# Performance work log

Hardware: AMD Instinct MI355X
Metric: run time of the kernel (lower is better)

The kernel has to match this reference:

```python
import jax, jax.numpy as jnp
import numpy as np

N_NODES = 50000
N_EDGES = 600000
D = 128
LN_EPS = 1e-5


def setup_inputs() -> dict:
    key = jax.random.key(0)
    ks = jax.random.split(key, 10)
    s = 1.0 / np.sqrt(D)
    return {
        "node_reps": jax.random.normal(ks[0], (N_NODES, D), jnp.float32),
        "edge_reps": jax.random.normal(ks[1], (N_EDGES, D), jnp.float32),
        "src_idx": jax.random.randint(ks[2], (N_EDGES,), 0, N_NODES, jnp.int32),
        "dst_idx": jnp.sort(jax.random.randint(ks[3], (N_EDGES,), 0, N_NODES, jnp.int32)),
        "Wq": jax.random.normal(ks[4], (D, D), jnp.float32) * s,
        "Wk": jax.random.normal(ks[5], (D, D), jnp.float32) * s,
        "Wv": jax.random.normal(ks[6], (D, D), jnp.float32) * s,
        "Wo": jax.random.normal(ks[7], (D, D), jnp.float32) * s,
        "ln_gamma": jnp.ones((D,), jnp.float32),
        "ln_beta": jnp.zeros((D,), jnp.float32),
        "W1": jax.random.normal(ks[8], (3 * D, D), jnp.float32) * (1.0 / np.sqrt(3 * D)),
        "b1": jnp.zeros((D,), jnp.float32),
        "W2": jax.random.normal(ks[9], (D, D), jnp.float32) * s,
        "b2": jnp.zeros((D,), jnp.float32),
    }


def _layer_norm(x, g, b):
    mu = jnp.mean(x, axis=-1, keepdims=True)
    var = jnp.mean(jnp.square(x - mu), axis=-1, keepdims=True)
    return (x - mu) * jax.lax.rsqrt(var + LN_EPS) * g + b


def reference(node_reps, edge_reps, src_idx, dst_idx, Wq, Wk, Wv, Wo,
              ln_gamma, ln_beta, W1, b1, W2, b2):
    n_nodes, d = node_reps.shape
    # dense projections once per node (kernel-friendly GEMMs)
    q = node_reps @ Wq                                  # [N, d]
    k_nodes = node_reps @ Wk                            # [N, d]
    v_nodes = node_reps @ Wv                            # [N, d]
    # per-edge gather + edge bias
    k_e = k_nodes[src_idx] + edge_reps                  # [E, d]
    scores = jnp.sum(q[dst_idx] * k_e, axis=-1) / jnp.sqrt(jnp.float32(d))  # [E]
    # segment softmax over edges sharing the same dst node
    seg_max = jax.ops.segment_max(scores, dst_idx, num_segments=n_nodes)
    ex = jnp.exp(scores - seg_max[dst_idx])
    denom = jax.ops.segment_sum(ex, dst_idx, num_segments=n_nodes)
    alpha = ex / denom[dst_idx]                          # [E]
    v_e = v_nodes[src_idx] + edge_reps                   # [E, d]
    agg = jax.ops.segment_sum(alpha[:, None] * v_e, dst_idx, num_segments=n_nodes)  # [N, d]
    updated = _layer_norm(node_reps + agg @ Wo, ln_gamma, ln_beta)  # [N, d]
    # triplet fusion MLP over (dst node, edge, src node)
    h_trip = jnp.concatenate([node_reps[dst_idx], edge_reps, node_reps[src_idx]], axis=-1)  # [E, 3d]
    fused = jax.nn.relu(h_trip @ W1 + b1) @ W2 + b2      # [E, d]
    return updated, fused
```

## Files before the change

### kernel.cpp

```cpp
#include <hip/hip_runtime.h>
#include <hip/hip_bf16.h>

#define NN 50000
#define NE 600000
#define D 128

typedef __bf16 bf16x8 __attribute__((ext_vector_type(8)));
typedef __bf16 bf16x4 __attribute__((ext_vector_type(4)));
typedef float f32x4 __attribute__((ext_vector_type(4)));


static __device__ __forceinline__ f32x4 bf4_to_f32(bf16x4 v) {
  f32x4 r;
  r[0] = (float)v[0]; r[1] = (float)v[1]; r[2] = (float)v[2]; r[3] = (float)v[3];
  return r;
}

static __device__ __forceinline__ void gload_lds16(const void* g, void* l) {
  __builtin_amdgcn_global_load_lds(
      (const __attribute__((address_space(1))) unsigned int*)g,
      (__attribute__((address_space(3))) unsigned int*)l, 16, 0, 0);
}

static __device__ __forceinline__ bf16x8 load_a_frag_nc(const float* __restrict__ A,
                                                        int row, int k0) {
  const f32x4* p = (const f32x4*)(A + (size_t)row * D + k0);
  f32x4 v0 = p[0], v1 = p[1];
  bf16x8 r;
  r[0] = (__bf16)v0[0]; r[1] = (__bf16)v0[1]; r[2] = (__bf16)v0[2]; r[3] = (__bf16)v0[3];
  r[4] = (__bf16)v1[0]; r[5] = (__bf16)v1[1]; r[6] = (__bf16)v1[2]; r[7] = (__bf16)v1[3];
  return r;
}

static __device__ __forceinline__ void stage_a_tile(const float* __restrict__ A, int M,
                                                    int row_base, char* lds, int tid) {
  const int l32 = tid & 31;
  const int g = tid >> 5;
#pragma unroll
  for (int it = 0; it < 16; ++it) {
    int rl = it * 8 + g;
    int r = row_base + rl;
    f32x4 v = {};
    if (r < M) v = *(const f32x4*)(A + (size_t)r * D + l32 * 4);
    bf16x4 b;
    b[0] = (__bf16)v[0]; b[1] = (__bf16)v[1]; b[2] = (__bf16)v[2]; b[3] = (__bf16)v[3];
    int byte = (rl * 256 + l32 * 8) ^ ((rl & 7) << 4);
    *(bf16x4*)(lds + byte) = b;
  }
}

static __device__ __forceinline__ bf16x8 read_a_frag(const char* lds, int rl, int k0) {
  int byte = (rl * 256 + k0 * 2) ^ ((rl & 7) << 4);
  return *(const bf16x8*)(lds + byte);
}

struct PrepArgs {
  const float* W[8];
  __bf16* WT[8];
  const int* dst;
  int* offs;
};

__global__ void prep_all(PrepArgs pa) {
  int b = blockIdx.x;
  if (b < 512) {
    int w = b >> 6;
    int t = (b & 63) * 256 + threadIdx.x;
    int n = t & 127, k = t >> 7;
    pa.WT[w][n * 128 + k] = (__bf16)pa.W[w][k * 128 + n];
  } else {
    int n = (b - 512) * 256 + threadIdx.x;
    if (n > NN) return;
    int lo = 0, hi = NE;
    while (lo < hi) {
      int mid = (lo + hi) >> 1;
      if (pa.dst[mid] < n) lo = mid + 1; else hi = mid;
    }
    pa.offs[n] = lo;
  }
}

struct GemmBatch {
  const __bf16* BT[5];
  void* C[5];
  const float* bias[5];
  int bf16out[5];
};

__global__ __launch_bounds__(256) void gemm_k128_b(const float* __restrict__ A,
                                                   GemmBatch gb, int M) {
  __shared__ __align__(16) char atile[128 * 256];
  const int y = blockIdx.y;
  const __bf16* __restrict__ BT = gb.BT[y];
  const int tid = threadIdx.x;
  const int lane = tid & 63;
  const int wave = tid >> 6;
  const int wr = wave >> 1, wc = wave & 1;
  const int row0 = blockIdx.x * 128;
  const int col0 = wc * 64;
  const int lr = lane & 15;
  const int lk = (lane >> 4) << 3;

  stage_a_tile(A, M, row0, atile, tid);
  __syncthreads();

  f32x4 acc[4][4] = {};
#pragma unroll
  for (int kk = 0; kk < 4; ++kk) {
    const int k0 = kk * 32 + lk;
    bf16x8 a[4], b[4];
#pragma unroll
    for (int m = 0; m < 4; ++m) a[m] = read_a_frag(atile, wr * 64 + m * 16 + lr, k0);
#pragma unroll
    for (int n = 0; n < 4; ++n) b[n] = *(const bf16x8*)(BT + (size_t)(col0 + n * 16 + lr) * D + k0);
#pragma unroll
    for (int m = 0; m < 4; ++m)
#pragma unroll
      for (int n = 0; n < 4; ++n)
        acc[m][n] = __builtin_amdgcn_mfma_f32_16x16x32_bf16(a[m], b[n], acc[m][n], 0, 0, 0);
  }
  const int rr = (lane >> 4) * 4;
  float bv[4] = {0.f, 0.f, 0.f, 0.f};
  if (gb.bias[y]) {
#pragma unroll
    for (int n = 0; n < 4; ++n) bv[n] = gb.bias[y][col0 + n * 16 + lr];
  }
  if (gb.bf16out[y]) {
    __bf16* __restrict__ C = (__bf16*)gb.C[y];
#pragma unroll
    for (int m = 0; m < 4; ++m)
#pragma unroll
      for (int j = 0; j < 4; ++j) {
        int r = row0 + wr * 64 + m * 16 + rr + j;
        if (r < M) {
#pragma unroll
          for (int n = 0; n < 4; ++n)
            C[(size_t)r * D + col0 + n * 16 + lr] = (__bf16)(acc[m][n][j] + bv[n]);
        }
      }
  } else {
    float* __restrict__ C = (float*)gb.C[y];
#pragma unroll
    for (int m = 0; m < 4; ++m)
#pragma unroll
      for (int j = 0; j < 4; ++j) {
        int r = row0 + wr * 64 + m * 16 + rr + j;
        if (r < M) {
#pragma unroll
          for (int n = 0; n < 4; ++n)
            C[(size_t)r * D + col0 + n * 16 + lr] = acc[m][n][j] + bv[n];
        }
      }
  }
}

__global__ __launch_bounds__(256) void fused_edge_attn(
    const float* __restrict__ edge,
    const __bf16* __restrict__ W1bT,
    const __bf16* __restrict__ W2T,
    const __bf16* __restrict__ P1,
    const __bf16* __restrict__ P3,
    const int* __restrict__ dst,
    const int* __restrict__ src,
    const float* __restrict__ b2,
    float* __restrict__ out_fused,
    const float* __restrict__ Q,
    const __bf16* __restrict__ K,
    const __bf16* __restrict__ V,
    const int* __restrict__ offs,
    const __bf16* __restrict__ WoT,
    const float* __restrict__ noderep,
    const float* __restrict__ gamma,
    const float* __restrict__ beta,
    float* __restrict__ out_updated) {
  __shared__ __align__(16) char bufA[64 * 256];
  __shared__ __align__(16) char bufB[64 * 256];
  const int tid = threadIdx.x;
  const int grp = blockIdx.x / 5;
  const int role = blockIdx.x % 5;

  if (role >= 2) {
    const int ebi = grp * 3 + (role - 2);
    const int eb = ebi * 64;
    const int lane = tid & 63;
    const int wave = tid >> 6;
    const int wr = wave >> 1, wc = wave & 1;
    const int lr = lane & 15;
    const int lk = (lane >> 4) << 3;
    const int col0 = wc * 64;

    {
      const int gr = lane >> 4;
      const int slot = lane & 15;
      int di[4], si[4];
#pragma unroll
      for (int c = 0; c < 4; ++c) {
        int rl = wave * 16 + c * 4 + gr;
        di[c] = dst[eb + rl];
        si[c] = src[eb + rl];
      }
#pragma unroll
      for (int c = 0; c < 4; ++c) {
        int rl = wave * 16 + c * 4 + gr;
        int sb = (slot * 16) ^ ((rl & 7) << 4);
        gload_lds16((const char*)(P1 + (size_t)di[c] * D) + sb,
                    bufA + (wave * 16 + c * 4) * 256);
        gload_lds16((const char*)(P3 + (size_t)si[c] * D) + sb,
                    bufB + (wave * 16 + c * 4) * 256);
      }
    }

    f32x4 acc[2][4] = {};
#pragma unroll
    for (int kk = 0; kk < 4; ++kk) {
      const int k0 = kk * 32 + lk;
      bf16x8 a[2], b[4];
#pragma unroll
      for (int m = 0; m < 2; ++m) a[m] = load_a_frag_nc(edge, eb + wr * 32 + m * 16 + lr, k0);
#pragma unroll
      for (int n = 0; n < 4; ++n) b[n] = *(const bf16x8*)(W1bT + (size_t)(col0 + n * 16 + lr) * D + k0);
#pragma unroll
      for (int m = 0; m < 2; ++m)
#pragma unroll
        for (int n = 0; n < 4; ++n)
          acc[m][n] = __builtin_amdgcn_mfma_f32_16x16x32_bf16(a[m], b[n], acc[m][n], 0, 0, 0);
    }
    __syncthreads();

    const int rr = (lane >> 4) * 4;
#pragma unroll
    for (int m = 0; m < 2; ++m) {
#pragma unroll
      for (int j = 0; j < 4; ++j) {
        int rl = wr * 32 + m * 16 + rr + j;
#pragma unroll
        for (int n = 0; n < 4; ++n) {
          int c = col0 + n * 16 + lr;
          int byte = (rl * 256 + c * 2) ^ ((rl & 7) << 4);
          float g1 = (float)*(const __bf16*)(bufA + byte);
          float g3 = (float)*(const __bf16*)(bufB + byte);
          float v = fmaxf(acc[m][n][j] + g1 + g3, 0.f);
          *(__bf16*)(bufA + byte) = (__bf16)v;
        }
      }
    }
    __syncthreads();

    float b2v[4];
#pragma unroll
    for (int n = 0; n < 4; ++n) b2v[n] = b2[col0 + n * 16 + lr];
    f32x4 acc2[2][4] = {};
#pragma unroll
    for (int kk = 0; kk < 4; ++kk) {
      const int k0 = kk * 32 + lk;
      bf16x8 a[2], b[4];
#pragma unroll
      for (int m = 0; m < 2; ++m) a[m] = read_a_frag(bufA, wr * 32 + m * 16 + lr, k0);
#pragma unroll
      for (int n = 0; n < 4; ++n) b[n] = *(const bf16x8*)(W2T + (size_t)(col0 + n * 16 + lr) * D + k0);
#pragma unroll
      for (int m = 0; m < 2; ++m)
#pragma unroll
        for (int n = 0; n < 4; ++n)
          acc2[m][n] = __builtin_amdgcn_mfma_f32_16x16x32_bf16(a[m], b[n], acc2[m][n], 0, 0, 0);
    }
#pragma unroll
    for (int m = 0; m < 2; ++m)
#pragma unroll
      for (int j = 0; j < 4; ++j) {
        int rl = wr * 32 + m * 16 + rr + j;
        int e = eb + rl;
#pragma unroll
        for (int n = 0; n < 4; ++n) {
          int c = col0 + n * 16 + lr;
          out_fused[(size_t)e * D + c] = acc2[m][n][j] + b2v[n];
        }
      }
  } else {
    const int nw = tid >> 5;
    int node = (grp * 2 + role) * 8 + nw;
    int l32 = tid & 31;
    int s0 = offs[node], s1 = offs[node + 1];
    int cnt = s1 - s0;
    f32x4 q = *(const f32x4*)(Q + (size_t)node * D + l32 * 4);
    float m = -__builtin_inff(), l = 0.f;
    f32x4 a = {0.f, 0.f, 0.f, 0.f};

    int si0 = 0, si1 = 0;
    bf16x4 kb0 = {}, vb0 = {};
    f32x4 ee0 = {};
    if (cnt > 0) si0 = src[s0];
    if (cnt > 1) si1 = src[s0 + 1];
    if (cnt > 0) {
      kb0 = *(const bf16x4*)(K + (size_t)si0 * D + l32 * 4);
      vb0 = *(const bf16x4*)(V + (size_t)si0 * D + l32 * 4);
      ee0 = *(const f32x4*)(edge + (size_t)s0 * D + l32 * 4);
    }
    for (int i = 0; i < cnt; ++i) {
      int si2 = 0;
      if (i + 2 < cnt) si2 = src[s0 + i + 2];
      bf16x4 kb1 = {}, vb1 = {};
      f32x4 ee1 = {};
      if (i + 1 < cnt) {
        kb1 = *(const bf16x4*)(K + (size_t)si1 * D + l32 * 4);
        vb1 = *(const bf16x4*)(V + (size_t)si1 * D + l32 * 4);
        ee1 = *(const f32x4*)(edge + (size_t)(s0 + i + 1) * D + l32 * 4);
      }
      f32x4 kpe = bf4_to_f32(kb0) + ee0;
      float part = q[0] * kpe[0] + q[1] * kpe[1] + q[2] * kpe[2] + q[3] * kpe[3];
#pragma unroll
      for (int off = 16; off >= 1; off >>= 1) part += __shfl_xor(part, off, 64);
      float s = part * 0.08838834764831845f;
      float mn = fmaxf(m, s);
      float sc = __expf(m - mn);
      float w = __expf(s - mn);
      l = l * sc + w;
      f32x4 vpe = bf4_to_f32(vb0) + ee0;
      a[0] = a[0] * sc + w * vpe[0];
      a[1] = a[1] * sc + w * vpe[1];
      a[2] = a[2] * sc + w * vpe[2];
      a[3] = a[3] * sc + w * vpe[3];
      m = mn;
      si0 = si1; si1 = si2;
      kb0 = kb1; vb0 = vb1; ee0 = ee1;
    }
    float inv = l > 0.f ? 1.f / l : 0.f;
    f32x4 r;
    r[0] = a[0] * inv; r[1] = a[1] * inv; r[2] = a[2] * inv; r[3] = a[3] * inv;

    {
      bf16x4 rb;
      rb[0] = (__bf16)r[0]; rb[1] = (__bf16)r[1];
      rb[2] = (__bf16)r[2]; rb[3] = (__bf16)r[3];
      int byte = (nw * 256 + l32 * 8) ^ ((nw & 7) << 4);
      *(bf16x4*)(bufA + byte) = rb;
    }
    __syncthreads();

    {
      const int wave = tid >> 6;
      const int lane = tid & 63;
      const int lr = lane & 15;
      const int lk = (lane >> 4) << 3;
      f32x4 acc[2] = {};
#pragma unroll
      for (int kk = 0; kk < 4; ++kk) {
        int k0 = kk * 32 + lk;
        bf16x8 af = read_a_frag(bufA, lr, k0);
#pragma unroll
        for (int t = 0; t < 2; ++t) {
          int n = wave * 2 + t;
          bf16x8 b = *(const bf16x8*)(WoT + (size_t)(n * 16 + lr) * D + k0);
          acc[t] = __builtin_amdgcn_mfma_f32_16x16x32_bf16(af, b, acc[t], 0, 0, 0);
        }
      }
      float* xl = (float*)bufB;
      const int rr = (lane >> 4) * 4;
      if (rr < 8) {
#pragma unroll
        for (int t = 0; t < 2; ++t) {
          int n = wave * 2 + t;
#pragma unroll
          for (int j = 0; j < 4; ++j)
            xl[(rr + j) * 128 + n * 16 + lr] = acc[t][j];
        }
      }
    }
    __syncthreads();

    {
      const float* xl = (const float*)bufB;
      f32x4 xv = *(const f32x4*)(xl + nw * 128 + l32 * 4);
      f32x4 nv = *(const f32x4*)(noderep + (size_t)node * D + l32 * 4);
      float x0 = xv[0] + nv[0], x1 = xv[1] + nv[1];
      float x2 = xv[2] + nv[2], x3 = xv[3] + nv[3];
      float s = x0 + x1 + x2 + x3;
#pragma unroll
      for (int off = 16; off >= 1; off >>= 1) s += __shfl_xor(s, off, 64);
      float mu = s * (1.f / 128.f);
      float d0 = x0 - mu, d1 = x1 - mu, d2 = x2 - mu, d3 = x3 - mu;
      float vv = d0 * d0 + d1 * d1 + d2 * d2 + d3 * d3;
#pragma unroll
      for (int off = 16; off >= 1; off >>= 1) vv += __shfl_xor(vv, off, 64);
      float rstd = rsqrtf(vv * (1.f / 128.f) + 1e-5f);
      f32x4 g = *(const f32x4*)(gamma + l32 * 4);
      f32x4 bb = *(const f32x4*)(beta + l32 * 4);
      f32x4 o;
      o[0] = d0 * rstd * g[0] + bb[0];
      o[1] = d1 * rstd * g[1] + bb[1];
      o[2] = d2 * rstd * g[2] + bb[2];
      o[3] = d3 * rstd * g[3] + bb[3];
      *(f32x4*)(out_updated + (size_t)node * D + l32 * 4) = o;
    }
  }
}

extern "C" void kernel_launch(void* const* d_in, const int* in_sizes, int n_in,
                              void* d_out, int out_size, void* d_ws, size_t ws_size,
                              hipStream_t stream) {
  const float* node = (const float*)d_in[0];
  const float* edge = (const float*)d_in[1];
  const int* src = (const int*)d_in[2];
  const int* dst = (const int*)d_in[3];
  const float* Wq = (const float*)d_in[4];
  const float* Wk = (const float*)d_in[5];
  const float* Wv = (const float*)d_in[6];
  const float* Wo = (const float*)d_in[7];
  const float* gamma = (const float*)d_in[8];
  const float* beta = (const float*)d_in[9];
  const float* W1 = (const float*)d_in[10];
  const float* b1 = (const float*)d_in[11];
  const float* W2 = (const float*)d_in[12];
  const float* b2 = (const float*)d_in[13];

  float* out_updated = (float*)d_out;
  float* out_fused = (float*)d_out + (size_t)NN * D;

  char* ws = (char*)d_ws;
  size_t o = 0;
  auto take = [&](size_t bytes) {
    char* p = ws + o;
    o = (o + bytes + 255) & ~(size_t)255;
    return p;
  };
  int* offs = (int*)take((NN + 1) * sizeof(int));
  __bf16* WqT = (__bf16*)take(128 * 128 * 2);
  __bf16* WkT = (__bf16*)take(128 * 128 * 2);
  __bf16* WvT = (__bf16*)take(128 * 128 * 2);
  __bf16* WoT = (__bf16*)take(128 * 128 * 2);
  __bf16* W1aT = (__bf16*)take(128 * 128 * 2);
  __bf16* W1bT = (__bf16*)take(128 * 128 * 2);
  __bf16* W1cT = (__bf16*)take(128 * 128 * 2);
  __bf16* W2T = (__bf16*)take(128 * 128 * 2);
  float* Qb = (float*)take((size_t)NN * D * 4);
  __bf16* Kb = (__bf16*)take((size_t)NN * D * 2);
  __bf16* Vb = (__bf16*)take((size_t)NN * D * 2);
  __bf16* P1b = (__bf16*)take((size_t)NN * D * 2);
  __bf16* P3b = (__bf16*)take((size_t)NN * D * 2);

  PrepArgs pa;
  pa.W[0] = Wq; pa.WT[0] = WqT;
  pa.W[1] = Wk; pa.WT[1] = WkT;
  pa.W[2] = Wv; pa.WT[2] = WvT;
  pa.W[3] = Wo; pa.WT[3] = WoT;
  pa.W[4] = W1; pa.WT[4] = W1aT;
  pa.W[5] = W1 + 128 * 128; pa.WT[5] = W1bT;
  pa.W[6] = W1 + 256 * 128; pa.WT[6] = W1cT;
  pa.W[7] = W2; pa.WT[7] = W2T;
  pa.dst = dst; pa.offs = offs;
  prep_all<<<512 + (NN + 256) / 256, 256, 0, stream>>>(pa);

  int gnode = (NN + 127) / 128;
  GemmBatch gb;
  gb.BT[0] = WqT;  gb.C[0] = Qb;  gb.bias[0] = nullptr; gb.bf16out[0] = 0;
  gb.BT[1] = WkT;  gb.C[1] = Kb;  gb.bias[1] = nullptr; gb.bf16out[1] = 1;
  gb.BT[2] = WvT;  gb.C[2] = Vb;  gb.bias[2] = nullptr; gb.bf16out[2] = 1;
  gb.BT[3] = W1aT; gb.C[3] = P1b; gb.bias[3] = b1;      gb.bf16out[3] = 1;
  gb.BT[4] = W1cT; gb.C[4] = P3b; gb.bias[4] = nullptr; gb.bf16out[4] = 1;
  gemm_k128_b<<<dim3(gnode, 5), 256, 0, stream>>>(node, gb, NN);

  fused_edge_attn<<<15625, 256, 0, stream>>>(edge, W1bT, W2T, P1b, P3b, dst, src,
                                             b2, out_fused, Qb, Kb, Vb, offs,
                                             WoT, node, gamma, beta, out_updated);
}
```

Measured before the change: 428.8 us.

## Fuse projection GEMMs per row tile, interleave K/V, shrink edge tiles, drop softmax max

The projection GEMM now loops over all five weight matrices inside one block using a 64-row A tile, instead of using one grid slice per weight. This reuses the staged activations and cuts redundant A loads. K and V are written interleaved into one buffer so each edge needs a single 16-byte gather, and the fused edge kernel uses 32-edge tiles with a swizzled 4-role block mapping, launch bounds of 8 blocks per CU, and DPP-based warp reductions. The online softmax no longer tracks a running max and exponentiates raw scores. That is cheaper but can overflow if scores grow large.

```diff
diff --git a/kernel.cpp b/kernel.cpp
--- a/kernel.cpp
+++ b/kernel.cpp
@@ -9,12 +9,6 @@
 typedef __bf16 bf16x4 __attribute__((ext_vector_type(4)));
 typedef float f32x4 __attribute__((ext_vector_type(4)));
 
-
-static __device__ __forceinline__ f32x4 bf4_to_f32(bf16x4 v) {
-  f32x4 r;
-  r[0] = (float)v[0]; r[1] = (float)v[1]; r[2] = (float)v[2]; r[3] = (float)v[3];
-  return r;
-}
 
 static __device__ __forceinline__ void gload_lds16(const void* g, void* l) {
   __builtin_amdgcn_global_load_lds(
@@ -32,12 +26,12 @@
   return r;
 }
 
-static __device__ __forceinline__ void stage_a_tile(const float* __restrict__ A, int M,
-                                                    int row_base, char* lds, int tid) {
+static __device__ __forceinline__ void stage_a_tile64(const float* __restrict__ A, int M,
+                                                      int row_base, char* lds, int tid) {
   const int l32 = tid & 31;
   const int g = tid >> 5;
 #pragma unroll
-  for (int it = 0; it < 16; ++it) {
+  for (int it = 0; it < 8; ++it) {
     int rl = it * 8 + g;
     int r = row_base + rl;
     f32x4 v = {};
@@ -52,6 +46,20 @@
 static __device__ __forceinline__ bf16x8 read_a_frag(const char* lds, int rl, int k0) {
   int byte = (rl * 256 + k0 * 2) ^ ((rl & 7) << 4);
   return *(const bf16x8*)(lds + byte);
+}
+
+template <int CTRL>
+static __device__ __forceinline__ float dpp_add(float x) {
+  int v = __builtin_amdgcn_update_dpp(0, __float_as_int(x), CTRL, 0xf, 0xf, true);
+  return x + __int_as_float(v);
+}
+
+static __device__ __forceinline__ float red32(float x) {
+  x = dpp_add<0xB1>(x);
+  x = dpp_add<0x4E>(x);
+  x = dpp_add<0x124>(x);
+  x = dpp_add<0x128>(x);
+  return x + __shfl_xor(x, 16, 64);
 }
 
 struct PrepArgs {
@@ -84,77 +92,74 @@
   const __bf16* BT[5];
   void* C[5];
   const float* bias[5];
-  int bf16out[5];
+  int mode[5];
 };
 
 __global__ __launch_bounds__(256) void gemm_k128_b(const float* __restrict__ A,
                                                    GemmBatch gb, int M) {
-  __shared__ __align__(16) char atile[128 * 256];
-  const int y = blockIdx.y;
-  const __bf16* __restrict__ BT = gb.BT[y];
+  __shared__ __align__(16) char atile[64 * 256];
   const int tid = threadIdx.x;
   const int lane = tid & 63;
   const int wave = tid >> 6;
   const int wr = wave >> 1, wc = wave & 1;
-  const int row0 = blockIdx.x * 128;
+  const int row0 = blockIdx.x * 64;
   const int col0 = wc * 64;
   const int lr = lane & 15;
   const int lk = (lane >> 4) << 3;
-
-  stage_a_tile(A, M, row0, atile, tid);
+  const int rr = (lane >> 4) * 4;
+
+  stage_a_tile64(A, M, row0, atile, tid);
   __syncthreads();
 
-  f32x4 acc[4][4] = {};
-#pragma unroll
-  for (int kk = 0; kk < 4; ++kk) {
-    const int k0 = kk * 32 + lk;
-    bf16x8 a[4], b[4];
-#pragma unroll
-    for (int m = 0; m < 4; ++m) a[m] = read_a_frag(atile, wr * 64 + m * 16 + lr, k0);
-#pragma unroll
-    for (int n = 0; n < 4; ++n) b[n] = *(const bf16x8*)(BT + (size_t)(col0 + n * 16 + lr) * D + k0);
-#pragma unroll
-    for (int m = 0; m < 4; ++m)
-#pragma unroll
-      for (int n = 0; n < 4; ++n)
-        acc[m][n] = __builtin_amdgcn_mfma_f32_16x16x32_bf16(a[m], b[n], acc[m][n], 0, 0, 0);
+#pragma unroll
+  for (int y = 0; y < 5; ++y) {
+    const __bf16* __restrict__ BT = gb.BT[y];
+    f32x4 acc[2][4] = {};
+#pragma unroll
+    for (int kk = 0; kk < 4; ++kk) {
+      const int k0 = kk * 32 + lk;
+      bf16x8 a[2], b[4];
+#pragma unroll
+      for (int m = 0; m < 2; ++m) a[m] = read_a_frag(atile, wr * 32 + m * 16 + lr, k0);
+#pragma unroll
+      for (int n = 0; n < 4; ++n) b[n] = *(const bf16x8*)(BT + (size_t)(col0 + n * 16 + lr) * D + k0);
+#pragma unroll
+      for (int m = 0; m < 2; ++m)
+#pragma unroll
+        for (int n = 0; n < 4; ++n)
+          acc[m][n] = __builtin_amdgcn_mfma_f32_16x16x32_bf16(a[m], b[n], acc[m][n], 0, 0, 0);
+    }
+    float bv[4] = {0.f, 0.f, 0.f, 0.f};
+    if (gb.bias[y]) {
+#pragma unroll
+      for (int n = 0; n < 4; ++n) bv[n] = gb.bias[y][col0 + n * 16 + lr];
+    }
+    const int mode = gb.mode[y];
+#pragma unroll
+    for (int m = 0; m < 2; ++m)
+#pragma unroll
+      for (int j = 0; j < 4; ++j) {
+        const int r = row0 + wr * 32 + m * 16 + rr + j;
+        if (r < M) {
+#pragma unroll
+          for (int n = 0; n < 4; ++n) {
+            const int c = col0 + n * 16 + lr;
+            const float val = acc[m][n][j] + bv[n];
+            if (mode == 0) {
+              ((float*)gb.C[y])[(size_t)r * D + c] = val;
+            } else if (mode == 1) {
+              ((__bf16*)gb.C[y])[(size_t)r * D + c] = (__bf16)val;
+            } else {
+              ((__bf16*)gb.C[y])[(size_t)r * 256 + (c >> 2) * 8 + (c & 3) + (mode == 3 ? 4 : 0)] =
+                  (__bf16)val;
+            }
+          }
+        }
+      }
   }
-  const int rr = (lane >> 4) * 4;
-  float bv[4] = {0.f, 0.f, 0.f, 0.f};
-  if (gb.bias[y]) {
-#pragma unroll
-    for (int n = 0; n < 4; ++n) bv[n] = gb.bias[y][col0 + n * 16 + lr];
-  }
-  if (gb.bf16out[y]) {
-    __bf16* __restrict__ C = (__bf16*)gb.C[y];
-#pragma unroll
-    for (int m = 0; m < 4; ++m)
-#pragma unroll
-      for (int j = 0; j < 4; ++j) {
-        int r = row0 + wr * 64 + m * 16 + rr + j;
-        if (r < M) {
-#pragma unroll
-          for (int n = 0; n < 4; ++n)
-            C[(size_t)r * D + col0 + n * 16 + lr] = (__bf16)(acc[m][n][j] + bv[n]);
-        }
-      }
-  } else {
-    float* __restrict__ C = (float*)gb.C[y];
-#pragma unroll
-    for (int m = 0; m < 4; ++m)
-#pragma unroll
-      for (int j = 0; j < 4; ++j) {
-        int r = row0 + wr * 64 + m * 16 + rr + j;
-        if (r < M) {
-#pragma unroll
-          for (int n = 0; n < 4; ++n)
-            C[(size_t)r * D + col0 + n * 16 + lr] = acc[m][n][j] + bv[n];
-        }
-      }
-  }
-}
-
-__global__ __launch_bounds__(256) void fused_edge_attn(
+}
+
+__global__ __launch_bounds__(256, 8) void fused_edge_attn(
     const float* __restrict__ edge,
     const __bf16* __restrict__ W1bT,
     const __bf16* __restrict__ W2T,
@@ -165,23 +170,24 @@
     const float* __restrict__ b2,
     float* __restrict__ out_fused,
     const float* __restrict__ Q,
-    const __bf16* __restrict__ K,
-    const __bf16* __restrict__ V,
+    const __bf16* __restrict__ KV,
     const int* __restrict__ offs,
     const __bf16* __restrict__ WoT,
     const float* __restrict__ noderep,
     const float* __restrict__ gamma,
     const float* __restrict__ beta,
     float* __restrict__ out_updated) {
-  __shared__ __align__(16) char bufA[64 * 256];
-  __shared__ __align__(16) char bufB[64 * 256];
+  __shared__ __align__(16) char bufA[32 * 256];
+  __shared__ __align__(16) char bufB[32 * 256];
   const int tid = threadIdx.x;
-  const int grp = blockIdx.x / 5;
-  const int role = blockIdx.x % 5;
-
-  if (role >= 2) {
-    const int ebi = grp * 3 + (role - 2);
-    const int eb = ebi * 64;
+  const int bid = blockIdx.x;
+  const int swz = (bid & 7) * 3125 + (bid >> 3);
+  const int grp = swz >> 2;
+  const int role = swz & 3;
+
+  if (role != 0) {
+    const int ebi = grp * 3 + (role - 1);
+    const int eb = ebi * 32;
     const int lane = tid & 63;
     const int wave = tid >> 6;
     const int wr = wave >> 1, wc = wave & 1;
@@ -192,56 +198,50 @@
     {
       const int gr = lane >> 4;
       const int slot = lane & 15;
-      int di[4], si[4];
-#pragma unroll
-      for (int c = 0; c < 4; ++c) {
-        int rl = wave * 16 + c * 4 + gr;
+      int di[2], sj[2];
+#pragma unroll
+      for (int c = 0; c < 2; ++c) {
+        int rl = wave * 8 + c * 4 + gr;
         di[c] = dst[eb + rl];
-        si[c] = src[eb + rl];
-      }
-#pragma unroll
-      for (int c = 0; c < 4; ++c) {
-        int rl = wave * 16 + c * 4 + gr;
+        sj[c] = src[eb + rl];
+      }
+#pragma unroll
+      for (int c = 0; c < 2; ++c) {
+        int rl = wave * 8 + c * 4 + gr;
         int sb = (slot * 16) ^ ((rl & 7) << 4);
         gload_lds16((const char*)(P1 + (size_t)di[c] * D) + sb,
-                    bufA + (wave * 16 + c * 4) * 256);
-        gload_lds16((const char*)(P3 + (size_t)si[c] * D) + sb,
-                    bufB + (wave * 16 + c * 4) * 256);
-      }
-    }
-
-    f32x4 acc[2][4] = {};
+                    bufA + (wave * 8 + c * 4) * 256);
+        gload_lds16((const char*)(P3 + (size_t)sj[c] * D) + sb,
+                    bufB + (wave * 8 + c * 4) * 256);
+      }
+    }
+
+    f32x4 acc[4] = {};
 #pragma unroll
     for (int kk = 0; kk < 4; ++kk) {
       const int k0 = kk * 32 + lk;
-      bf16x8 a[2], b[4];
-#pragma unroll
-      for (int m = 0; m < 2; ++m) a[m] = load_a_frag_nc(edge, eb + wr * 32 + m * 16 + lr, k0);
+      bf16x8 av = load_a_frag_nc(edge, eb + wr * 16 + lr, k0);
+      bf16x8 b[4];
 #pragma unroll
       for (int n = 0; n < 4; ++n) b[n] = *(const bf16x8*)(W1bT + (size_t)(col0 + n * 16 + lr) * D + k0);
 #pragma unroll
-      for (int m = 0; m < 2; ++m)
-#pragma unroll
-        for (int n = 0; n < 4; ++n)
-          acc[m][n] = __builtin_amdgcn_mfma_f32_16x16x32_bf16(a[m], b[n], acc[m][n], 0, 0, 0);
+      for (int n = 0; n < 4; ++n)
+        acc[n] = __builtin_amdgcn_mfma_f32_16x16x32_bf16(av, b[n], acc[n], 0, 0, 0);
     }
     __syncthreads();
 
     const int rr = (lane >> 4) * 4;
 #pragma unroll
-    for (int m = 0; m < 2; ++m) {
-#pragma unroll
-      for (int j = 0; j < 4; ++j) {
-        int rl = wr * 32 + m * 16 + rr + j;
-#pragma unroll
-        for (int n = 0; n < 4; ++n) {
-          int c = col0 + n * 16 + lr;
-          int byte = (rl * 256 + c * 2) ^ ((rl & 7) << 4);
-          float g1 = (float)*(const __bf16*)(bufA + byte);
-          float g3 = (float)*(const __bf16*)(bufB + byte);
-          float v = fmaxf(acc[m][n][j] + g1 + g3, 0.f);
-          *(__bf16*)(bufA + byte) = (__bf16)v;
-        }
+    for (int j = 0; j < 4; ++j) {
+      int rl = wr * 16 + rr + j;
+#pragma unroll
+      for (int n = 0; n < 4; ++n) {
+        int c = col0 + n * 16 + lr;
+        int byte = (rl * 256 + c * 2) ^ ((rl & 7) << 4);
+        float g1 = (float)*(const __bf16*)(bufA + byte);
+        float g3 = (float)*(const __bf16*)(bufB + byte);
+        float v = fmaxf(acc[n][j] + g1 + g3, 0.f);
+        *(__bf16*)(bufA + byte) = (__bf16)v;
       }
     }
     __syncthreads();
@@ -249,80 +249,71 @@
     float b2v[4];
 #pragma unroll
     for (int n = 0; n < 4; ++n) b2v[n] = b2[col0 + n * 16 + lr];
-    f32x4 acc2[2][4] = {};
+    f32x4 acc2[4] = {};
 #pragma unroll
     for (int kk = 0; kk < 4; ++kk) {
       const int k0 = kk * 32 + lk;
-      bf16x8 a[2], b[4];
-#pragma unroll
-      for (int m = 0; m < 2; ++m) a[m] = read_a_frag(bufA, wr * 32 + m * 16 + lr, k0);
+      bf16x8 av = read_a_frag(bufA, wr * 16 + lr, k0);
+      bf16x8 b[4];
 #pragma unroll
       for (int n = 0; n < 4; ++n) b[n] = *(const bf16x8*)(W2T + (size_t)(col0 + n * 16 + lr) * D + k0);
 #pragma unroll
-      for (int m = 0; m < 2; ++m)
-#pragma unroll
-        for (int n = 0; n < 4; ++n)
-          acc2[m][n] = __builtin_amdgcn_mfma_f32_16x16x32_bf16(a[m], b[n], acc2[m][n], 0, 0, 0);
-    }
-#pragma unroll
-    for (int m = 0; m < 2; ++m)
-#pragma unroll
-      for (int j = 0; j < 4; ++j) {
-        int rl = wr * 32 + m * 16 + rr + j;
-        int e = eb + rl;
-#pragma unroll
-        for (int n = 0; n < 4; ++n) {
-          int c = col0 + n * 16 + lr;
-          out_fused[(size_t)e * D + c] = acc2[m][n][j] + b2v[n];
-        }
-      }
+      for (int n = 0; n < 4; ++n)
+        acc2[n] = __builtin_amdgcn_mfma_f32_16x16x32_bf16(av, b[n], acc2[n], 0, 0, 0);
+    }
+#pragma unroll
+    for (int j = 0; j < 4; ++j) {
+      int rl = wr * 16 + rr + j;
+      int e = eb + rl;
+#pragma unroll
+      for (int n = 0; n < 4; ++n) {
+        int c = col0 + n * 16 + lr;
+        out_fused[(size_t)e * D + c] = acc2[n][j] + b2v[n];
+      }
+    }
   } else {
     const int nw = tid >> 5;
-    int node = (grp * 2 + role) * 8 + nw;
-    int l32 = tid & 31;
+    const int node = grp * 8 + nw;
+    const int l32 = tid & 31;
     int s0 = offs[node], s1 = offs[node + 1];
     int cnt = s1 - s0;
     f32x4 q = *(const f32x4*)(Q + (size_t)node * D + l32 * 4);
-    float m = -__builtin_inff(), l = 0.f;
+    float l = 0.f;
     f32x4 a = {0.f, 0.f, 0.f, 0.f};
 
     int si0 = 0, si1 = 0;
-    bf16x4 kb0 = {}, vb0 = {};
+    bf16x8 kv0 = {};
     f32x4 ee0 = {};
     if (cnt > 0) si0 = src[s0];
     if (cnt > 1) si1 = src[s0 + 1];
     if (cnt > 0) {
-      kb0 = *(const bf16x4*)(K + (size_t)si0 * D + l32 * 4);
-      vb0 = *(const bf16x4*)(V + (size_t)si0 * D + l32 * 4);
+      kv0 = *(const bf16x8*)(KV + (size_t)si0 * 256 + l32 * 8);
       ee0 = *(const f32x4*)(edge + (size_t)s0 * D + l32 * 4);
     }
     for (int i = 0; i < cnt; ++i) {
       int si2 = 0;
       if (i + 2 < cnt) si2 = src[s0 + i + 2];
-      bf16x4 kb1 = {}, vb1 = {};
+      bf16x8 kv1 = {};
       f32x4 ee1 = {};
       if (i + 1 < cnt) {
-        kb1 = *(const bf16x4*)(K + (size_t)si1 * D + l32 * 4);
-        vb1 = *(const bf16x4*)(V + (size_t)si1 * D + l32 * 4);
+        kv1 = *(const bf16x8*)(KV + (size_t)si1 * 256 + l32 * 8);
         ee1 = *(const f32x4*)(edge + (size_t)(s0 + i + 1) * D + l32 * 4);
       }
-      f32x4 kpe = bf4_to_f32(kb0) + ee0;
-      float part = q[0] * kpe[0] + q[1] * kpe[1] + q[2] * kpe[2] + q[3] * kpe[3];
-#pragma unroll
-      for (int off = 16; off >= 1; off >>= 1) part += __shfl_xor(part, off, 64);
-      float s = part * 0.08838834764831845f;
-      float mn = fmaxf(m, s);
-      float sc = __expf(m - mn);
-      float w = __expf(s - mn);
-      l = l * sc + w;
-      f32x4 vpe = bf4_to_f32(vb0) + ee0;
-      a[0] = a[0] * sc + w * vpe[0];
-      a[1] = a[1] * sc + w * vpe[1];
-      a[2] = a[2] * sc + w * vpe[2];
-      a[3] = a[3] * sc + w * vpe[3];
-      m = mn;
+      float k0f = (float)kv0[0] + ee0[0];
+      float k1f = (float)kv0[1] + ee0[1];
+      float k2f = (float)kv0[2] + ee0[2];
+      float k3f = (float)kv0[3] + ee0[3];
+      float p01 = fmaf(q[1], k1f, q[0] * k0f);
+      float p23 = fmaf(q[3], k3f, q[2] * k2f);
+      float s = red32(p01 + p23) * 0.08838834764831845f;
+      float w = __expf(s);
+      l += w;
+      a[0] = fmaf(w, (float)kv0[4] + ee0[0], a[0]);
+      a[1] = fmaf(w, (float)kv0[5] + ee0[1], a[1]);
+      a[2] = fmaf(w, (float)kv0[6] + ee0[2], a[2]);
+      a[3] = fmaf(w, (float)kv0[7] + ee0[3], a[3]);
       si0 = si1; si1 = si2;
-      kb0 = kb1; vb0 = vb1; ee0 = ee1;
+      kv0 = kv1; ee0 = ee1;
     }
     float inv = l > 0.f ? 1.f / l : 0.f;
     f32x4 r;
@@ -374,14 +365,10 @@
       f32x4 nv = *(const f32x4*)(noderep + (size_t)node * D + l32 * 4);
       float x0 = xv[0] + nv[0], x1 = xv[1] + nv[1];
       float x2 = xv[2] + nv[2], x3 = xv[3] + nv[3];
-      float s = x0 + x1 + x2 + x3;
-#pragma unroll
-      for (int off = 16; off >= 1; off >>= 1) s += __shfl_xor(s, off, 64);
+      float s = red32(x0 + x1 + x2 + x3);
       float mu = s * (1.f / 128.f);
       float d0 = x0 - mu, d1 = x1 - mu, d2 = x2 - mu, d3 = x3 - mu;
-      float vv = d0 * d0 + d1 * d1 + d2 * d2 + d3 * d3;
-#pragma unroll
-      for (int off = 16; off >= 1; off >>= 1) vv += __shfl_xor(vv, off, 64);
+      float vv = red32(d0 * d0 + d1 * d1 + d2 * d2 + d3 * d3);
       float rstd = rsqrtf(vv * (1.f / 128.f) + 1e-5f);
       f32x4 g = *(const f32x4*)(gamma + l32 * 4);
       f32x4 bb = *(const f32x4*)(beta + l32 * 4);
@@ -433,8 +420,7 @@
   __bf16* W1cT = (__bf16*)take(128 * 128 * 2);
   __bf16* W2T = (__bf16*)take(128 * 128 * 2);
   float* Qb = (float*)take((size_t)NN * D * 4);
-  __bf16* Kb = (__bf16*)take((size_t)NN * D * 2);
-  __bf16* Vb = (__bf16*)take((size_t)NN * D * 2);
+  __bf16* KVb = (__bf16*)take((size_t)NN * 256 * 2);
   __bf16* P1b = (__bf16*)take((size_t)NN * D * 2);
   __bf16* P3b = (__bf16*)take((size_t)NN * D * 2);
 
@@ -450,16 +436,15 @@
   pa.dst = dst; pa.offs = offs;
   prep_all<<<512 + (NN + 256) / 256, 256, 0, stream>>>(pa);
 
-  int gnode = (NN + 127) / 128;
   GemmBatch gb;
-  gb.BT[0] = WqT;  gb.C[0] = Qb;  gb.bias[0] = nullptr; gb.bf16out[0] = 0;
-  gb.BT[1] = WkT;  gb.C[1] = Kb;  gb.bias[1] = nullptr; gb.bf16out[1] = 1;
-  gb.BT[2] = WvT;  gb.C[2] = Vb;  gb.bias[2] = nullptr; gb.bf16out[2] = 1;
-  gb.BT[3] = W1aT; gb.C[3] = P1b; gb.bias[3] = b1;      gb.bf16out[3] = 1;
-  gb.BT[4] = W1cT; gb.C[4] = P3b; gb.bias[4] = nullptr; gb.bf16out[4] = 1;
-  gemm_k128_b<<<dim3(gnode, 5), 256, 0, stream>>>(node, gb, NN);
-
-  fused_edge_attn<<<15625, 256, 0, stream>>>(edge, W1bT, W2T, P1b, P3b, dst, src,
-                                             b2, out_fused, Qb, Kb, Vb, offs,
+  gb.BT[0] = WqT;  gb.C[0] = Qb;  gb.bias[0] = nullptr; gb.mode[0] = 0;
+  gb.BT[1] = WkT;  gb.C[1] = KVb; gb.bias[1] = nullptr; gb.mode[1] = 2;
+  gb.BT[2] = WvT;  gb.C[2] = KVb; gb.bias[2] = nullptr; gb.mode[2] = 3;
+  gb.BT[3] = W1aT; gb.C[3] = P1b; gb.bias[3] = b1;      gb.mode[3] = 1;
+  gb.BT[4] = W1cT; gb.C[4] = P3b; gb.bias[4] = nullptr; gb.mode[4] = 1;
+  gemm_k128_b<<<(NN + 63) / 64, 256, 0, stream>>>(node, gb, NN);
+
+  fused_edge_attn<<<25000, 256, 0, stream>>>(edge, W1bT, W2T, P1b, P3b, dst, src,
+                                             b2, out_fused, Qb, KVb, offs,
                                              WoT, node, gamma, beta, out_updated);
 }
```

Result: slower. 571.5 us (+33.3%).
